# Kernel optimization log

Hardware: AMD Instinct MI355X
Metric: run time of the kernel (lower is better)

## Reference

```python
import jax, jax.numpy as jnp
import numpy as np

DIM = 512
NUM_HEADS = 8
HEAD_DIM = DIM // NUM_HEADS


def setup_inputs() -> dict:
    key = jax.random.key(0)
    ks = jax.random.split(key, 9)
    s = 1.0 / np.sqrt(DIM)
    x = jax.random.normal(ks[0], (2, 4096, DIM), dtype=jnp.float32)
    Wq = jax.random.uniform(ks[1], (DIM, DIM), jnp.float32, -s, s)
    bq = jax.random.uniform(ks[2], (DIM,), jnp.float32, -s, s)
    Wk = jax.random.uniform(ks[3], (DIM, DIM), jnp.float32, -s, s)
    bk = jax.random.uniform(ks[4], (DIM,), jnp.float32, -s, s)
    Wv = jax.random.uniform(ks[5], (DIM, DIM), jnp.float32, -s, s)
    bv = jax.random.uniform(ks[6], (DIM,), jnp.float32, -s, s)
    Wo = jax.random.uniform(ks[7], (DIM, DIM), jnp.float32, -s, s)
    bo = jax.random.uniform(ks[8], (DIM,), jnp.float32, -s, s)
    return {"x": x, "Wq": Wq, "bq": bq, "Wk": Wk, "bk": bk,
            "Wv": Wv, "bv": bv, "Wo": Wo, "bo": bo}


def reference(x, Wq, bq, Wk, bk, Wv, bv, Wo, bo):
    B, S, D = x.shape
    H, Hd = NUM_HEADS, HEAD_DIM
    # Linear layers (torch stores weight as [out,in]; here W is [in,out])
    q = (x @ Wq + bq).reshape(B, S, H, Hd).transpose(0, 2, 1, 3)  # [B,H,S,Hd]
    k = (x @ Wk + bk).reshape(B, S, H, Hd).transpose(0, 2, 1, 3)
    v = (x @ Wv + bv).reshape(B, S, H, Hd).transpose(0, 2, 1, 3)
    # NOTE: original scales by dim**0.5, not head_dim**0.5
    energy = jnp.einsum('bhqd,bhkd->bhqk', q, k) / jnp.sqrt(jnp.float32(D))
    attn = jax.nn.softmax(energy, axis=-1)
    out = jnp.einsum('bhqk,bhkd->bhqd', attn, v)
    out = out.transpose(0, 2, 1, 3).reshape(B, S, D)
    return out @ Wo + bo
```

## Files before the change

kernel.cpp:

```cpp
#include <hip/hip_runtime.h>

typedef unsigned short USH;
typedef short s16x8 __attribute__((ext_vector_type(8)));
typedef float f32x4 __attribute__((ext_vector_type(4)));
typedef float f32x4v __attribute__((ext_vector_type(4)));
typedef unsigned int u32x4 __attribute__((ext_vector_type(4)));
typedef s16x8 s16x8_a __attribute__((may_alias));
typedef f32x4v f32x4v_a __attribute__((may_alias));
typedef u32x4 u32x4_a __attribute__((may_alias));
typedef unsigned long long u64_a __attribute__((may_alias));

#if __has_builtin(__builtin_amdgcn_exp2f)
#define EXP2F(x) __builtin_amdgcn_exp2f(x)
#else
#define EXP2F(x) __builtin_exp2f(x)
#endif

__device__ __forceinline__ USH f2bf(float f) {
  union { float f; unsigned int i; } c; c.f = f;
  unsigned int x = c.i;
  return (USH)((x + 0x7FFFu + ((x >> 16) & 1u)) >> 16);
}
__device__ __forceinline__ unsigned int pk_bf16(float a, float b) {
#if __has_builtin(__builtin_amdgcn_cvt_pk_bf16_f32)
  typedef USH ush2 __attribute__((ext_vector_type(2)));
  union { ush2 v; unsigned int u; } r;
  r.v = __builtin_amdgcn_cvt_pk_bf16_f32(a, b);
  return r.u;
#else
  union { float f; unsigned int i; } ca, cb; ca.f = a; cb.f = b;
  return ((ca.i + 0x8000u) >> 16) | ((cb.i + 0x8000u) & 0xFFFF0000u);
#endif
}

__device__ __forceinline__ f32x4 mfma16(s16x8 a, s16x8 b, f32x4 c) {
  return __builtin_amdgcn_mfma_f32_16x16x32_bf16(a, b, c, 0, 0, 0);
}

#if __has_builtin(__builtin_amdgcn_global_load_lds)
__device__ __forceinline__ void gld_lds16(const USH* g, USH* l) {
  __builtin_amdgcn_global_load_lds(
      static_cast<const unsigned int __attribute__((address_space(1)))*>(
          (const void __attribute__((address_space(1)))*)g),
      static_cast<unsigned int __attribute__((address_space(3)))*>(
          (void __attribute__((address_space(3)))*)l),
      16, 0, 0);
}
#else
__device__ __forceinline__ void gld_lds16(const USH* g, USH* l) {
  *(s16x8_a*)l = *(const s16x8_a*)g;
}
#endif

__global__ __launch_bounds__(256) void prep(
    const float* __restrict__ Wq, const float* __restrict__ Wk,
    const float* __restrict__ Wv, const float* __restrict__ Wo,
    const float* __restrict__ x, USH* __restrict__ wsT, USH* __restrict__ xb) {
  __shared__ float tile[32][33];
  const int z = blockIdx.z;
  const int t = threadIdx.x;
  if (z == 4) {
    const size_t b0 = ((size_t)blockIdx.y * 16 + blockIdx.x) * 16384;
    #pragma unroll
    for (int j = 0; j < 8; ++j) {
      const size_t i = b0 + (size_t)j * 2048 + t * 8;
      const f32x4v a = *(const f32x4v_a*)(x + i);
      const f32x4v b = *(const f32x4v_a*)(x + i + 4);
      u32x4 s;
      s.x = pk_bf16(a.x, a.y); s.y = pk_bf16(a.z, a.w);
      s.z = pk_bf16(b.x, b.y); s.w = pk_bf16(b.z, b.w);
      *(u32x4_a*)(xb + i) = s;
    }
    return;
  }
  const float* W = (z == 0) ? Wq : (z == 1) ? Wk : (z == 2) ? Wv : Wo;
  USH* WT = wsT + (size_t)z * 262144;
  const int n0 = blockIdx.x * 32, k0 = blockIdx.y * 32;
  const int tx = t & 31, ty = t >> 5;
  #pragma unroll
  for (int i = 0; i < 4; ++i)
    tile[ty + i * 8][tx] = W[(size_t)(k0 + ty + i * 8) * 512 + n0 + tx];
  __syncthreads();
  #pragma unroll
  for (int i = 0; i < 4; ++i)
    WT[(size_t)(n0 + ty + i * 8) * 512 + k0 + tx] = f2bf(tile[tx][ty + i * 8]);
}

template <int MODE>
__global__ __launch_bounds__(256, 3) void gemm_bias(
    const USH* __restrict__ A, const USH* __restrict__ BT0,
    const float* __restrict__ b0, const float* __restrict__ b1,
    const float* __restrict__ b2,
    USH* __restrict__ oQ, USH* __restrict__ oKV, float* __restrict__ oF) {
  __shared__ __align__(16) USH As[128 * 68];
  __shared__ __align__(16) USH Bs[128 * 68];
  const int z = blockIdx.z;
  const USH* BT = BT0 + (size_t)z * 262144;
  const float* bias = (z == 0) ? b0 : ((z == 1) ? b1 : b2);
  USH* outb = (z == 0) ? oQ : (oKV + (size_t)(z - 1) * 4194304);
  const float qs = (MODE == 1 && z == 0) ? 0.06375871528132839f : 1.0f;

  const int t = threadIdx.x;
  const int w = t >> 6, lane = t & 63;
  const int c = lane & 15, g = lane >> 4;
  const int wm = w & 1, wn = w >> 1;
  const int m0 = blockIdx.x * 128, n0 = blockIdx.y * 128;
  const int srow = t >> 1, scol = (t & 1) * 32;

  f32x4 acc[4][4] = {};

  const USH* Ap0 = A + (size_t)(m0 + srow) * 512 + scol;
  const USH* Bp0 = BT + (size_t)(n0 + srow) * 512 + scol;
  s16x8 pa[4], pb[4];
  #pragma unroll
  for (int j = 0; j < 4; ++j) {
    pa[j] = *(const s16x8_a*)(Ap0 + j * 8);
    pb[j] = *(const s16x8_a*)(Bp0 + j * 8);
  }

  for (int kt = 0; kt < 8; ++kt) {
    __syncthreads();
    #pragma unroll
    for (int j = 0; j < 4; ++j) {
      *(s16x8_a*)(As + srow * 68 + scol + j * 8) = pa[j];
      *(s16x8_a*)(Bs + srow * 68 + scol + j * 8) = pb[j];
    }
    const int ktn = (kt < 7) ? kt + 1 : kt;
    #pragma unroll
    for (int j = 0; j < 4; ++j) {
      pa[j] = *(const s16x8_a*)(Ap0 + ktn * 64 + j * 8);
      pb[j] = *(const s16x8_a*)(Bp0 + ktn * 64 + j * 8);
    }
    __syncthreads();
    #pragma unroll
    for (int ks = 0; ks < 2; ++ks) {
      s16x8 af[4], bfr[4];
      #pragma unroll
      for (int i = 0; i < 4; ++i) {
        af[i]  = *(const s16x8_a*)(As + (wm * 64 + i * 16 + c) * 68 + ks * 32 + g * 8);
        bfr[i] = *(const s16x8_a*)(Bs + (wn * 64 + i * 16 + c) * 68 + ks * 32 + g * 8);
      }
      #pragma unroll
      for (int mf = 0; mf < 4; ++mf)
        #pragma unroll
        for (int nf = 0; nf < 4; ++nf)
          acc[mf][nf] = mfma16(af[mf], bfr[nf], acc[mf][nf]);
    }
  }

  #pragma unroll
  for (int nf = 0; nf < 4; ++nf) {
    const int n = n0 + wn * 64 + nf * 16 + c;
    const float bv = bias[n];
    #pragma unroll
    for (int mf = 0; mf < 4; ++mf)
      #pragma unroll
      for (int r = 0; r < 4; ++r) {
        const int m = m0 + wm * 64 + mf * 16 + g * 4 + r;
        const float v = (acc[mf][nf][r] + bv) * qs;
        if (MODE == 0) {
          oF[(size_t)m * 512 + n] = v;
        } else {
          const int bb = m >> 12, s = m & 4095, h = n >> 6, hd = n & 63;
          if (z == 2)
            outb[(((size_t)(bb * 8 + h)) * 64 + hd) * 4096 + s] = f2bf(v);
          else
            outb[(((size_t)(bb * 8 + h)) * 4096 + s) * 64 + hd] = f2bf(v);
        }
      }
  }
}

__global__ __launch_bounds__(256, 2) void attn(const USH* __restrict__ Qbuf,
                                               const USH* __restrict__ kv,
                                               USH* __restrict__ att) {
  __shared__ __align__(16) USH Ks[2 * 4096];
  __shared__ __align__(16) USH Vt[2 * 4096];
  __shared__ __align__(16) USH Ps[4][32 * 76];
  __shared__ float lbuf[4][32];

  const int t = threadIdx.x;
  const int w = t >> 6, lane = t & 63;
  const int c = lane & 15, g = lane >> 4;
  const int linear = blockIdx.x + (blockIdx.y << 5);
  const int xcd = linear & 7, idx = linear >> 3;
  const int bh = xcd + ((idx >> 5) << 3);
  const int bb = bh >> 3, hh = bh & 7;
  const size_t base = (size_t)bh * 262144;
  const USH* Q = Qbuf + base;
  const USH* K = kv + base;
  const USH* V = kv + 4194304 + base;
  const int q0 = (idx & 31) * 128 + w * 32;

  s16x8 qf[2][2];
  #pragma unroll
  for (int qi = 0; qi < 2; ++qi)
    #pragma unroll
    for (int kh = 0; kh < 2; ++kh)
      qf[qi][kh] = *(const s16x8_a*)(Q + (size_t)(q0 + qi * 16 + c) * 64 + kh * 32 + g * 8);

  s16x8 onesf;
  {
    const short one = (short)0x3F80, val = (c == 0) ? one : (short)0;
    #pragma unroll
    for (int j = 0; j < 8; ++j) onesf[j] = val;
  }

  f32x4 o[2][4] = {};
  f32x4 o_l[2] = {};

  const int keyK = w * 16 + (lane >> 2);
  const int ccK = (lane & 3) ^ ((keyK >> 1) & 3);
  const USH* gK0 = K + (size_t)keyK * 64 + ccK * 8;
  const int hdV = w * 8 + (lane >> 3);
  const int ccV = (lane & 7) ^ (hdV & 7);
  const USH* gV0 = V + (size_t)hdV * 4096 + ccV * 8;
  USH* lK = Ks + w * 512 + lane * 8;
  USH* lV = Vt + w * 512 + lane * 8;

  #pragma unroll
  for (int j = 0; j < 2; ++j) {
    gld_lds16(gK0 + j * 32, lK + j * 2048);
    gld_lds16(gV0 + (size_t)j * 131072, lV + j * 2048);
  }

  for (int kt = 0; kt < 64; ++kt) {
    const int buf = kt & 1;
    __syncthreads();
    if (kt < 63) {
      const int nb = (buf ^ 1) * 4096;
      #pragma unroll
      for (int j = 0; j < 2; ++j) {
        gld_lds16(gK0 + (size_t)(kt + 1) * 4096 + j * 32, lK + nb + j * 2048);
        gld_lds16(gV0 + (size_t)(kt + 1) * 64 + (size_t)j * 131072, lV + nb + j * 2048);
      }
    }

    f32x4 st[2][4] = {};
    #pragma unroll
    for (int kh = 0; kh < 2; ++kh) {
      s16x8 ak[4];
      #pragma unroll
      for (int kff = 0; kff < 4; ++kff) {
        const int row = kff * 16 + c;
        const int qsw = (g ^ ((c >> 1) & 3)) * 8;
        ak[kff] = *(const s16x8_a*)(Ks + buf * 4096 + kh * 2048 + row * 32 + qsw);
      }
      #pragma unroll
      for (int qi = 0; qi < 2; ++qi)
        #pragma unroll
        for (int kff = 0; kff < 4; ++kff)
          st[qi][kff] = mfma16(ak[kff], qf[qi][kh], st[qi][kff]);
    }

    #pragma unroll
    for (int qi = 0; qi < 2; ++qi)
      #pragma unroll
      for (int kff = 0; kff < 4; ++kff)
        #pragma unroll
        for (int r = 0; r < 4; ++r)
          st[qi][kff][r] = EXP2F(st[qi][kff][r]);

    #pragma unroll
    for (int qi = 0; qi < 2; ++qi)
      #pragma unroll
      for (int kff = 0; kff < 4; ++kff) {
        const unsigned int lo = pk_bf16(st[qi][kff][0], st[qi][kff][1]);
        const unsigned int hi = pk_bf16(st[qi][kff][2], st[qi][kff][3]);
        *(u64_a*)(&Ps[w][(qi * 16 + c) * 76 + kff * 16 + g * 4]) =
            (unsigned long long)lo | ((unsigned long long)hi << 32);
      }

    #pragma unroll
    for (int kf = 0; kf < 2; ++kf) {
      s16x8 ap[2];
      #pragma unroll
      for (int qi = 0; qi < 2; ++qi)
        ap[qi] = *(const s16x8_a*)(&Ps[w][(qi * 16 + c) * 76 + kf * 32 + g * 8]);
      s16x8 bv[4];
      #pragma unroll
      for (int hf = 0; hf < 4; ++hf) {
        const int qv = ((kf * 4 + g) ^ (c & 7)) * 8;
        bv[hf] = *(const s16x8_a*)(Vt + buf * 4096 + (c + 16 * hf) * 64 + qv);
      }
      #pragma unroll
      for (int qi = 0; qi < 2; ++qi) {
        #pragma unroll
        for (int hf = 0; hf < 4; ++hf)
          o[qi][hf] = mfma16(ap[qi], bv[hf], o[qi][hf]);
        o_l[qi] = mfma16(ap[qi], onesf, o_l[qi]);
      }
    }
  }

  if (c == 0) {
    #pragma unroll
    for (int qi = 0; qi < 2; ++qi)
      #pragma unroll
      for (int r = 0; r < 4; ++r) lbuf[w][qi * 16 + g * 4 + r] = o_l[qi][r];
  }
  __syncthreads();

  #pragma unroll
  for (int qi = 0; qi < 2; ++qi)
    #pragma unroll
    for (int r = 0; r < 4; ++r) {
      const int ml = qi * 16 + g * 4 + r;
      const float linv = 1.0f / lbuf[w][ml];
      const int qrow = q0 + ml;
      #pragma unroll
      for (int hf = 0; hf < 4; ++hf) {
        const int hd = c + 16 * hf;
        att[((size_t)(bb * 4096 + qrow)) * 512 + hh * 64 + hd] =
            f2bf(o[qi][hf][r] * linv);
      }
    }
}

extern "C" void kernel_launch(void* const* d_in, const int* in_sizes, int n_in,
                              void* d_out, int out_size, void* d_ws, size_t ws_size,
                              hipStream_t stream) {
  (void)in_sizes; (void)n_in; (void)out_size; (void)ws_size;
  const float* x  = (const float*)d_in[0];
  const float* Wq = (const float*)d_in[1];
  const float* bq = (const float*)d_in[2];
  const float* Wk = (const float*)d_in[3];
  const float* bk = (const float*)d_in[4];
  const float* Wv = (const float*)d_in[5];
  const float* bv = (const float*)d_in[6];
  const float* Wo = (const float*)d_in[7];
  const float* bo = (const float*)d_in[8];
  USH* ws  = (USH*)d_ws;
  USH* wT  = ws;
  USH* kv  = ws + 1048576;
  USH* att = ws + 1048576 + 8388608;
  float* outF = (float*)d_out;
  USH* qscratch = (USH*)d_out;
  USH* xb = (USH*)d_out + 4194304;

  prep<<<dim3(16, 16, 5), 256, 0, stream>>>(Wq, Wk, Wv, Wo, x, wT, xb);
  gemm_bias<1><<<dim3(64, 4, 3), 256, 0, stream>>>(xb, wT, bq, bk, bv,
                                                   qscratch, kv, nullptr);
  attn<<<dim3(32, 16), 256, 0, stream>>>(qscratch, kv, att);
  gemm_bias<0><<<dim3(64, 4, 1), 256, 0, stream>>>(att, wT + 3 * 262144, bo, bo, bo,
                                                   nullptr, nullptr, outF);
}
```

Before: 210.0 us.

## Software-pipeline attention loop: overlap next tile's QK with current softmax·V

Restructures the attention main loop into a two-stage software pipeline. The QK^T MFMAs for tile kt+1 are issued alongside the exp/pack/PV work for tile kt, using alternating score registers stA and stB. V gets a triple-buffered LDS ring so a tile's V stays resident for one extra iteration while the next is being loaded. The aim is to hide MFMA and exp latency by interleaving independent work, at the cost of more LDS and more live registers, which could lower occupancy or cause spills.

```diff
diff --git a/kernel.cpp b/kernel.cpp
--- a/kernel.cpp
+++ b/kernel.cpp
@@ -175,7 +175,7 @@
                                                const USH* __restrict__ kv,
                                                USH* __restrict__ att) {
   __shared__ __align__(16) USH Ks[2 * 4096];
-  __shared__ __align__(16) USH Vt[2 * 4096];
+  __shared__ __align__(16) USH Vt[3 * 4096];
   __shared__ __align__(16) USH Ps[4][32 * 76];
   __shared__ float lbuf[4][32];
 
@@ -208,6 +208,7 @@
 
   f32x4 o[2][4] = {};
   f32x4 o_l[2] = {};
+  const f32x4 kZero = {0.f, 0.f, 0.f, 0.f};
 
   const int keyK = w * 16 + (lane >> 2);
   const int ccK = (lane & 3) ^ ((keyK >> 1) & 3);
@@ -218,59 +219,52 @@
   USH* lK = Ks + w * 512 + lane * 8;
   USH* lV = Vt + w * 512 + lane * 8;
 
-  #pragma unroll
-  for (int j = 0; j < 2; ++j) {
-    gld_lds16(gK0 + j * 32, lK + j * 2048);
-    gld_lds16(gV0 + (size_t)j * 131072, lV + j * 2048);
-  }
-
-  for (int kt = 0; kt < 64; ++kt) {
-    const int buf = kt & 1;
-    __syncthreads();
-    if (kt < 63) {
-      const int nb = (buf ^ 1) * 4096;
-      #pragma unroll
-      for (int j = 0; j < 2; ++j) {
-        gld_lds16(gK0 + (size_t)(kt + 1) * 4096 + j * 32, lK + nb + j * 2048);
-        gld_lds16(gV0 + (size_t)(kt + 1) * 64 + (size_t)j * 131072, lV + nb + j * 2048);
-      }
-    }
-
-    f32x4 st[2][4] = {};
-    #pragma unroll
-    for (int kh = 0; kh < 2; ++kh) {
-      s16x8 ak[4];
+  auto DMA = [&](int kt, int kOff, int vOff) {
+    #pragma unroll
+    for (int j = 0; j < 2; ++j) {
+      gld_lds16(gK0 + (size_t)kt * 4096 + j * 32, lK + kOff + j * 2048);
+      gld_lds16(gV0 + (size_t)kt * 64 + (size_t)j * 131072, lV + vOff + j * 2048);
+    }
+  };
+
+  auto QK = [&](int kbase, f32x4 (&st)[2][4]) {
+    s16x8 ak[4];
+    #pragma unroll
+    for (int kff = 0; kff < 4; ++kff) {
+      const int row = kff * 16 + c;
+      const int qsw = (g ^ ((c >> 1) & 3)) * 8;
+      ak[kff] = *(const s16x8_a*)(Ks + kbase + row * 32 + qsw);
+    }
+    #pragma unroll
+    for (int qi = 0; qi < 2; ++qi)
+      #pragma unroll
+      for (int kff = 0; kff < 4; ++kff)
+        st[qi][kff] = mfma16(ak[kff], qf[qi][0], kZero);
+    #pragma unroll
+    for (int kff = 0; kff < 4; ++kff) {
+      const int row = kff * 16 + c;
+      const int qsw = (g ^ ((c >> 1) & 3)) * 8;
+      ak[kff] = *(const s16x8_a*)(Ks + kbase + 2048 + row * 32 + qsw);
+    }
+    #pragma unroll
+    for (int qi = 0; qi < 2; ++qi)
+      #pragma unroll
+      for (int kff = 0; kff < 4; ++kff)
+        st[qi][kff] = mfma16(ak[kff], qf[qi][1], st[qi][kff]);
+  };
+
+  auto SMPV = [&](f32x4 (&st)[2][4], int vbase) {
+    #pragma unroll
+    for (int qi = 0; qi < 2; ++qi)
       #pragma unroll
       for (int kff = 0; kff < 4; ++kff) {
-        const int row = kff * 16 + c;
-        const int qsw = (g ^ ((c >> 1) & 3)) * 8;
-        ak[kff] = *(const s16x8_a*)(Ks + buf * 4096 + kh * 2048 + row * 32 + qsw);
-      }
-      #pragma unroll
-      for (int qi = 0; qi < 2; ++qi)
         #pragma unroll
-        for (int kff = 0; kff < 4; ++kff)
-          st[qi][kff] = mfma16(ak[kff], qf[qi][kh], st[qi][kff]);
-    }
-
-    #pragma unroll
-    for (int qi = 0; qi < 2; ++qi)
-      #pragma unroll
-      for (int kff = 0; kff < 4; ++kff)
-        #pragma unroll
-        for (int r = 0; r < 4; ++r)
-          st[qi][kff][r] = EXP2F(st[qi][kff][r]);
-
-    #pragma unroll
-    for (int qi = 0; qi < 2; ++qi)
-      #pragma unroll
-      for (int kff = 0; kff < 4; ++kff) {
+        for (int r = 0; r < 4; ++r) st[qi][kff][r] = EXP2F(st[qi][kff][r]);
         const unsigned int lo = pk_bf16(st[qi][kff][0], st[qi][kff][1]);
         const unsigned int hi = pk_bf16(st[qi][kff][2], st[qi][kff][3]);
         *(u64_a*)(&Ps[w][(qi * 16 + c) * 76 + kff * 16 + g * 4]) =
             (unsigned long long)lo | ((unsigned long long)hi << 32);
       }
-
     #pragma unroll
     for (int kf = 0; kf < 2; ++kf) {
       s16x8 ap[2];
@@ -281,7 +275,7 @@
       #pragma unroll
       for (int hf = 0; hf < 4; ++hf) {
         const int qv = ((kf * 4 + g) ^ (c & 7)) * 8;
-        bv[hf] = *(const s16x8_a*)(Vt + buf * 4096 + (c + 16 * hf) * 64 + qv);
+        bv[hf] = *(const s16x8_a*)(Vt + vbase + (c + 16 * hf) * 64 + qv);
       }
       #pragma unroll
       for (int qi = 0; qi < 2; ++qi) {
@@ -291,7 +285,36 @@
         o_l[qi] = mfma16(ap[qi], onesf, o_l[qi]);
       }
     }
-  }
+  };
+
+  f32x4 stA[2][4], stB[2][4];
+
+  DMA(0, 0, 0);
+  __syncthreads();
+  DMA(1, 4096, 4096);
+  QK(0, stA);
+  int vD = 8192;
+  int vP = 0;
+
+  for (int j = 0; j < 31; ++j) {
+    __syncthreads();
+    DMA(2 * j + 2, 0, vD);
+    QK(4096, stB);
+    SMPV(stA, vP);
+    vD = (vD == 8192) ? 0 : vD + 4096;
+    vP = (vP == 8192) ? 0 : vP + 4096;
+    __syncthreads();
+    DMA(2 * j + 3, 4096, vD);
+    QK(0, stA);
+    SMPV(stB, vP);
+    vD = (vD == 8192) ? 0 : vD + 4096;
+    vP = (vP == 8192) ? 0 : vP + 4096;
+  }
+  __syncthreads();
+  QK(4096, stB);
+  SMPV(stA, vP);
+  vP = (vP == 8192) ? 0 : vP + 4096;
+  SMPV(stB, vP);
 
   if (c == 0) {
     #pragma unroll
```

New measurement: 214.5 us. 2.2% more time.

## Triple-buffer K/V tiles in attention with partial vmcnt waits

Applied to the files above, without the earlier changes.

Moves the attention loop's K/V staging from double to triple buffering in LDS. Each iteration now prefetches the tile two steps ahead and waits only until the current tile's loads are done, using an explicit s_waitcnt vmcnt(4) plus barrier instead of a full __syncthreads. This is meant to hide global-load latency better. The cost is more LDS per block (about 48KB K/V plus the P buffers), which may limit two blocks per CU. It also relies on the ordering of vmcnt counters in inline asm.

```diff
diff --git a/kernel.cpp b/kernel.cpp
--- a/kernel.cpp
+++ b/kernel.cpp
@@ -174,8 +174,8 @@
 __global__ __launch_bounds__(256, 2) void attn(const USH* __restrict__ Qbuf,
                                                const USH* __restrict__ kv,
                                                USH* __restrict__ att) {
-  __shared__ __align__(16) USH Ks[2 * 4096];
-  __shared__ __align__(16) USH Vt[2 * 4096];
+  __shared__ __align__(16) USH Ks[3 * 4096];
+  __shared__ __align__(16) USH Vt[3 * 4096];
   __shared__ __align__(16) USH Ps[4][32 * 76];
   __shared__ float lbuf[4][32];
 
@@ -218,24 +218,15 @@
   USH* lK = Ks + w * 512 + lane * 8;
   USH* lV = Vt + w * 512 + lane * 8;
 
-  #pragma unroll
-  for (int j = 0; j < 2; ++j) {
-    gld_lds16(gK0 + j * 32, lK + j * 2048);
-    gld_lds16(gV0 + (size_t)j * 131072, lV + j * 2048);
-  }
-
-  for (int kt = 0; kt < 64; ++kt) {
-    const int buf = kt & 1;
-    __syncthreads();
-    if (kt < 63) {
-      const int nb = (buf ^ 1) * 4096;
-      #pragma unroll
-      for (int j = 0; j < 2; ++j) {
-        gld_lds16(gK0 + (size_t)(kt + 1) * 4096 + j * 32, lK + nb + j * 2048);
-        gld_lds16(gV0 + (size_t)(kt + 1) * 64 + (size_t)j * 131072, lV + nb + j * 2048);
-      }
-    }
-
+  auto DMA = [&](int kt, int slotOff) {
+    #pragma unroll
+    for (int j = 0; j < 2; ++j) {
+      gld_lds16(gK0 + (size_t)kt * 4096 + j * 32, lK + slotOff + j * 2048);
+      gld_lds16(gV0 + (size_t)kt * 64 + (size_t)j * 131072, lV + slotOff + j * 2048);
+    }
+  };
+
+  auto STEP = [&](int sb) {
     f32x4 st[2][4] = {};
     #pragma unroll
     for (int kh = 0; kh < 2; ++kh) {
@@ -244,7 +235,7 @@
       for (int kff = 0; kff < 4; ++kff) {
         const int row = kff * 16 + c;
         const int qsw = (g ^ ((c >> 1) & 3)) * 8;
-        ak[kff] = *(const s16x8_a*)(Ks + buf * 4096 + kh * 2048 + row * 32 + qsw);
+        ak[kff] = *(const s16x8_a*)(Ks + sb + kh * 2048 + row * 32 + qsw);
       }
       #pragma unroll
       for (int qi = 0; qi < 2; ++qi)
@@ -252,25 +243,17 @@
         for (int kff = 0; kff < 4; ++kff)
           st[qi][kff] = mfma16(ak[kff], qf[qi][kh], st[qi][kff]);
     }
-
     #pragma unroll
     for (int qi = 0; qi < 2; ++qi)
       #pragma unroll
-      for (int kff = 0; kff < 4; ++kff)
+      for (int kff = 0; kff < 4; ++kff) {
         #pragma unroll
-        for (int r = 0; r < 4; ++r)
-          st[qi][kff][r] = EXP2F(st[qi][kff][r]);
-
-    #pragma unroll
-    for (int qi = 0; qi < 2; ++qi)
-      #pragma unroll
-      for (int kff = 0; kff < 4; ++kff) {
+        for (int r = 0; r < 4; ++r) st[qi][kff][r] = EXP2F(st[qi][kff][r]);
         const unsigned int lo = pk_bf16(st[qi][kff][0], st[qi][kff][1]);
         const unsigned int hi = pk_bf16(st[qi][kff][2], st[qi][kff][3]);
         *(u64_a*)(&Ps[w][(qi * 16 + c) * 76 + kff * 16 + g * 4]) =
             (unsigned long long)lo | ((unsigned long long)hi << 32);
       }
-
     #pragma unroll
     for (int kf = 0; kf < 2; ++kf) {
       s16x8 ap[2];
@@ -281,7 +264,7 @@
       #pragma unroll
       for (int hf = 0; hf < 4; ++hf) {
         const int qv = ((kf * 4 + g) ^ (c & 7)) * 8;
-        bv[hf] = *(const s16x8_a*)(Vt + buf * 4096 + (c + 16 * hf) * 64 + qv);
+        bv[hf] = *(const s16x8_a*)(Vt + sb + (c + 16 * hf) * 64 + qv);
       }
       #pragma unroll
       for (int qi = 0; qi < 2; ++qi) {
@@ -291,7 +274,23 @@
         o_l[qi] = mfma16(ap[qi], onesf, o_l[qi]);
       }
     }
-  }
+  };
+
+  DMA(0, 0);
+  DMA(1, 4096);
+  int sCur = 0, sNext = 4096, sFree = 8192;
+
+  for (int kt = 0; kt < 62; ++kt) {
+    asm volatile("s_waitcnt vmcnt(4)\n\ts_barrier" ::: "memory");
+    DMA(kt + 2, sFree);
+    STEP(sCur);
+    const int tmp = sCur; sCur = sNext; sNext = sFree; sFree = tmp;
+  }
+  asm volatile("s_waitcnt vmcnt(4)\n\ts_barrier" ::: "memory");
+  STEP(sCur);
+  { const int tmp = sCur; sCur = sNext; sNext = sFree; sFree = tmp; }
+  asm volatile("s_waitcnt vmcnt(0)\n\ts_barrier" ::: "memory");
+  STEP(sCur);
 
   if (c == 0) {
     #pragma unroll
```

Result: no change. 210.7 us (+0.3%).
